# Kernel tuning notes

Hardware: AMD Instinct MI355X
Metric: run time of the kernel (lower is better)

## Reference

```python
import jax, jax.numpy as jnp
import numpy as np

B, T, C, N = 4, 1024, 960, 64
H = C // N
R_W, R_A, R_V, R_G = 64, 64, 32, 128
LN_EPS = 0.00064


def setup_inputs() -> dict:
    key = jax.random.key(0)
    ks = jax.random.split(key, 28)
    s = 0.5 / np.sqrt(C)
    u = lambda k, sh, sc: jax.random.uniform(k, sh, jnp.float32, -sc, sc)
    n = lambda k, sh, sc: jax.random.normal(k, sh, jnp.float32) * sc
    return {
        "x": jax.random.normal(ks[0], (B, T, C), jnp.float32),
        "v_first": jax.random.normal(ks[1], (B, T, C), jnp.float32),
        "x_r": jax.random.uniform(ks[2], (1, 1, C), jnp.float32),
        "x_w": jax.random.uniform(ks[3], (1, 1, C), jnp.float32),
        "x_k": jax.random.uniform(ks[4], (1, 1, C), jnp.float32),
        "x_v": jax.random.uniform(ks[5], (1, 1, C), jnp.float32),
        "x_a": jax.random.uniform(ks[6], (1, 1, C), jnp.float32),
        "x_g": jax.random.uniform(ks[7], (1, 1, C), jnp.float32),
        "w0": n(ks[8], (1, 1, C), 0.5) - 2.0,
        "w1": n(ks[9], (C, R_W), 0.02),
        "w2": n(ks[10], (R_W, C), 0.02),
        "a0": n(ks[11], (1, 1, C), 0.3),
        "a1": n(ks[12], (C, R_A), 0.02),
        "a2": n(ks[13], (R_A, C), 0.02),
        "v0": n(ks[14], (1, 1, C), 0.3) + 0.73,
        "v1": n(ks[15], (C, R_V), 0.02),
        "v2": n(ks[16], (R_V, C), 0.02),
        "g1": n(ks[17], (C, R_G), 0.02),
        "g2": n(ks[18], (R_G, C), 0.02),
        "k_k": n(ks[19], (1, 1, C), 0.1) + 0.71,
        "k_a": n(ks[20], (1, 1, C), 0.1) + 1.02,
        "r_k": n(ks[21], (H, N), 0.1) - 0.04,
        "Wr": u(ks[22], (C, C), s),
        "Wk": u(ks[23], (C, C), 0.1 * s),
        "Wv": u(ks[24], (C, C), s),
        "Wo": u(ks[25], (C, C), s),
        "ln_g": jnp.ones((C,), jnp.float32),
        "ln_b": jnp.zeros((C,), jnp.float32),
    }


def reference(x, v_first, x_r, x_w, x_k, x_v, x_a, x_g, w0, w1, w2,
              a0, a1, a2, v0, v1, v2, g1, g2, k_k, k_a, r_k,
              Wr, Wk, Wv, Wo, ln_g, ln_b):
    Bx, Tx, Cx = x.shape
    # token shift: xx[t] = x[t-1] - x[t], with x[-1] = 0
    xx = jnp.concatenate([jnp.zeros_like(x[:, :1]), x[:, :-1]], axis=1) - x
    xr = x + xx * x_r; xw = x + xx * x_w; xk = x + xx * x_k
    xv = x + xx * x_v; xa = x + xx * x_a; xg = x + xx * x_g
    r = xr @ Wr
    w_raw = w0 + jnp.tanh(xw @ w1) @ w2       # log-space decay
    k = xk @ Wk
    v = xv @ Wv
    # layer_id > 0: residual mix with layer-0 value
    v = v + (v_first - v) * jax.nn.sigmoid(v0 + (xv @ v1) @ v2)
    a = jax.nn.sigmoid(a0 + (xa @ a1) @ a2)   # in-context learning rate
    g = jax.nn.sigmoid(xg @ g1) @ g2          # gate
    kk = (k * k_k).reshape(Bx, Tx, H, N)
    kk = kk / jnp.maximum(jnp.linalg.norm(kk, axis=-1, keepdims=True), 1e-12)
    k = k * (1.0 + (a - 1.0) * k_a)
    f32 = jnp.float32
    rh = r.reshape(Bx, Tx, H, N).astype(f32)
    kh = k.reshape(Bx, Tx, H, N).astype(f32)
    vh = v.reshape(Bx, Tx, H, N).astype(f32)
    wh = jnp.exp(-jax.nn.softplus(-w_raw.reshape(Bx, Tx, H, N).astype(f32)) - 0.5)
    ah = (-kk).astype(f32)                              # removal key
    bh = (kk * a.reshape(Bx, Tx, H, N)).astype(f32)     # replacement key

    def step(state, inp):
        r_t, w_t, k_t, v_t, a_t, b_t = inp  # each (B,H,N); state (B,H,N,N)
        sa = jnp.einsum('bhij,bhj->bhi', state, a_t)
        state = (state * w_t[:, :, None, :]
                 + sa[..., None] * b_t[:, :, None, :]
                 + v_t[..., None] * k_t[:, :, None, :])
        out_t = jnp.einsum('bhij,bhj->bhi', state, r_t)
        return state, out_t

    tm = lambda u: jnp.transpose(u, (1, 0, 2, 3))  # time-major
    state0 = jnp.zeros((Bx, H, N, N), f32)
    _, wkv = jax.lax.scan(step, state0, (tm(rh), tm(wh), tm(kh), tm(vh), tm(ah), tm(bh)))
    wkv = jnp.transpose(wkv, (1, 0, 2, 3))  # (B,T,H,N)
    # GroupNorm with H groups == per-head layernorm over N
    mu = wkv.mean(-1, keepdims=True)
    var = wkv.var(-1, keepdims=True)
    xn = (wkv - mu) / jnp.sqrt(var + LN_EPS)
    xn = xn * ln_g.reshape(H, N) + ln_b.reshape(H, N)
    bonus = (rh * kh * r_k).sum(-1, keepdims=True) * vh  # r*k*v bonus term
    xo = (xn + bonus).astype(x.dtype).reshape(Bx, Tx, Cx)
    return (xo * g) @ Wo


if __name__ == "__main__":
    out = reference(**setup_inputs())
    print(out.shape, out.dtype)
```

## Files before the change

kernel.cpp:

```cpp
#include <hip/hip_runtime.h>
#include <hip/hip_bf16.h>
#include <math.h>

#define Tn 1024
#define Cn 960
#define Hn 15
#define Nn 64
#define Mn 4096

typedef short bf16x8 __attribute__((ext_vector_type(8)));
typedef float f32x4 __attribute__((ext_vector_type(4)));

#define MCc ((size_t)Mn * Cn)

__device__ __forceinline__ float sigmf(float x) { return 1.0f / (1.0f + __expf(-x)); }

__device__ __forceinline__ ushort f2bf(float x) {
    unsigned u = __float_as_uint(x);
    unsigned r = (u + 0x7FFFu + ((u >> 16) & 1u)) >> 16;
    return (ushort)r;
}
__device__ __forceinline__ float bf2f(ushort h) { return __uint_as_float(((unsigned)h) << 16); }

__device__ __forceinline__ float rowsum16(float x) {
    x += __int_as_float(__builtin_amdgcn_update_dpp(0, __float_as_int(x), 0x121, 0xF, 0xF, true));
    x += __int_as_float(__builtin_amdgcn_update_dpp(0, __float_as_int(x), 0x122, 0xF, 0xF, true));
    x += __int_as_float(__builtin_amdgcn_update_dpp(0, __float_as_int(x), 0x124, 0xF, 0xF, true));
    x += __int_as_float(__builtin_amdgcn_update_dpp(0, __float_as_int(x), 0x128, 0xF, 0xF, true));
    return x;
}

__global__ __launch_bounds__(256) void mix6_kernel(
    const float* __restrict__ x,
    const float* __restrict__ mr, const float* __restrict__ mw, const float* __restrict__ mk,
    const float* __restrict__ mv, const float* __restrict__ ma, const float* __restrict__ mg,
    ushort* __restrict__ r_sp, ushort* __restrict__ w_sp, ushort* __restrict__ k_sp,
    ushort* __restrict__ v_sp, ushort* __restrict__ a_sp, ushort* __restrict__ g_sp)
{
    int idx = blockIdx.x * 256 + threadIdx.x;
    int e = idx * 4;
    if (e >= Mn * Cn) return;
    int m = e / Cn;
    int c = e - m * Cn;
    int t = m & (Tn - 1);
    float4 xv = *(const float4*)(x + e);
    float4 xp = make_float4(0.f, 0.f, 0.f, 0.f);
    if (t > 0) xp = *(const float4*)(x + e - Cn);
    float4 dx = make_float4(xp.x - xv.x, xp.y - xv.y, xp.z - xv.z, xp.w - xv.w);
#define MIXSPLIT(MIXP, P)                                                     \
    {                                                                         \
        float4 mm = *(const float4*)(MIXP + c);                               \
        float4 O = make_float4(xv.x + dx.x * mm.x, xv.y + dx.y * mm.y,        \
                               xv.z + dx.z * mm.z, xv.w + dx.w * mm.w);       \
        ushort h0 = f2bf(O.x), h1 = f2bf(O.y), h2 = f2bf(O.z), h3 = f2bf(O.w);\
        ushort l0 = f2bf(O.x - bf2f(h0)), l1 = f2bf(O.y - bf2f(h1));          \
        ushort l2 = f2bf(O.z - bf2f(h2)), l3 = f2bf(O.w - bf2f(h3));          \
        *(ushort4*)(P + e) = make_ushort4(h0, h1, h2, h3);                    \
        *(ushort4*)(P + MCc + e) = make_ushort4(l0, l1, l2, l3);              \
    }
    MIXSPLIT(mr, r_sp)
    MIXSPLIT(mw, w_sp)
    MIXSPLIT(mk, k_sp)
    MIXSPLIT(mv, v_sp)
    MIXSPLIT(ma, a_sp)
    MIXSPLIT(mg, g_sp)
#undef MIXSPLIT
}

__global__ __launch_bounds__(256) void convWT_kernel(
    const float* __restrict__ W, ushort* __restrict__ Thi, ushort* __restrict__ Tlo)
{
    __shared__ float tile[32][33];
    int k0 = blockIdx.x * 32, n0 = blockIdx.y * 32;
    int tx = threadIdx.x & 31, ty = threadIdx.x >> 5;
#pragma unroll
    for (int i = 0; i < 4; ++i)
        tile[ty + 8 * i][tx] = W[(size_t)(k0 + ty + 8 * i) * 960 + n0 + tx];
    __syncthreads();
#pragma unroll
    for (int i = 0; i < 4; ++i) {
        float x = tile[tx][ty + 8 * i];
        ushort h = f2bf(x);
        ushort l = f2bf(x - bf2f(h));
        size_t o = (size_t)(n0 + ty + 8 * i) * 960 + k0 + tx;
        Thi[o] = h;
        Tlo[o] = l;
    }
}

__global__ __launch_bounds__(256) void wprep_kernel(
    const float* __restrict__ w1, const float* __restrict__ a1,
    const float* __restrict__ v1, const float* __restrict__ g1,
    const float* __restrict__ w2, const float* __restrict__ a2,
    const float* __restrict__ v2, const float* __restrict__ g2,
    ushort* __restrict__ arena)
{
    __shared__ float tile[32][33];
    int z = blockIdx.z;
    const float* src;
    int K, N;
    size_t off;
    switch (z) {
        case 0: src = w1; K = 960; N = 64;  off = 0;      break;
        case 1: src = a1; K = 960; N = 64;  off = 122880; break;
        case 2: src = v1; K = 960; N = 32;  off = 245760; break;
        case 3: src = g1; K = 960; N = 128; off = 307200; break;
        case 4: src = w2; K = 64;  N = 960; off = 552960; break;
        case 5: src = a2; K = 64;  N = 960; off = 675840; break;
        case 6: src = v2; K = 32;  N = 960; off = 798720; break;
        default: src = g2; K = 128; N = 960; off = 860160; break;
    }
    int k0 = blockIdx.x * 32, n0 = blockIdx.y * 32;
    if (k0 >= K || n0 >= N) return;
    int tx = threadIdx.x & 31, ty = threadIdx.x >> 5;
#pragma unroll
    for (int i = 0; i < 4; ++i)
        tile[ty + 8 * i][tx] = src[(size_t)(k0 + ty + 8 * i) * N + n0 + tx];
    __syncthreads();
    ushort* Thi = arena + off;
    ushort* Tlo = arena + off + (size_t)K * N;
#pragma unroll
    for (int i = 0; i < 4; ++i) {
        float x = tile[tx][ty + 8 * i];
        ushort h = f2bf(x);
        ushort l = f2bf(x - bf2f(h));
        size_t o = (size_t)(n0 + ty + 8 * i) * K + k0 + tx;
        Thi[o] = h;
        Tlo[o] = l;
    }
}

__global__ __launch_bounds__(256) void convN_kernel(
    const float* __restrict__ X, ushort* __restrict__ hi, ushort* __restrict__ lo, int n4)
{
    int idx = blockIdx.x * 256 + threadIdx.x;
    if (idx >= n4) return;
    int e = idx * 4;
    float4 x = *(const float4*)(X + e);
    ushort h0 = f2bf(x.x), h1 = f2bf(x.y), h2 = f2bf(x.z), h3 = f2bf(x.w);
    ushort l0 = f2bf(x.x - bf2f(h0)), l1 = f2bf(x.y - bf2f(h1));
    ushort l2 = f2bf(x.z - bf2f(h2)), l3 = f2bf(x.w - bf2f(h3));
    *(ushort4*)(hi + e) = make_ushort4(h0, h1, h2, h3);
    *(ushort4*)(lo + e) = make_ushort4(l0, l1, l2, l3);
}

__global__ __launch_bounds__(512) void gemm_bf3_kernel(
    const ushort* __restrict__ Ahi, const ushort* __restrict__ Alo,
    const ushort* __restrict__ Bhi, const ushort* __restrict__ Blo,
    float* __restrict__ C, int ldc)
{
    __shared__ __align__(16) ushort sA[2][2][128][40];
    __shared__ __align__(16) ushort sB[2][2][64][40];
    const int K = 960;
    int bm = blockIdx.x * 128, bn = blockIdx.y * 64;
    int t = threadIdx.x;
    int w = t >> 6, l = t & 63;
    int lr = l & 15, lk = l >> 4;

    int ar = t >> 2, aseg = t & 3;
    int brr = t >> 2;
    int bhl = brr >> 6, brow = brr & 63, bseg = t & 3;
    const ushort* gAh = Ahi + (size_t)(bm + ar) * K + aseg * 8;
    const ushort* gAl = Alo + (size_t)(bm + ar) * K + aseg * 8;
    const ushort* gB = (bhl ? Blo : Bhi) + (size_t)(bn + brow) * K + bseg * 8;

    f32x4 acc[4];
#pragma unroll
    for (int j = 0; j < 4; ++j)
#pragma unroll
        for (int e = 0; e < 4; ++e) acc[j][e] = 0.f;

    float4 rhP, rlP, rbP, rhQ, rlQ, rbQ;
#define LOADP(KOFF)                                                           \
    {                                                                         \
        rhP = *(const float4*)(gAh + (KOFF));                                 \
        rlP = *(const float4*)(gAl + (KOFF));                                 \
        rbP = *(const float4*)(gB + (KOFF));                                  \
    }
#define LOADQ(KOFF)                                                           \
    {                                                                         \
        rhQ = *(const float4*)(gAh + (KOFF));                                 \
        rlQ = *(const float4*)(gAl + (KOFF));                                 \
        rbQ = *(const float4*)(gB + (KOFF));                                  \
    }
#define WRITEP(BUF)                                                           \
    {                                                                         \
        *(float4*)&sA[BUF][0][ar][aseg * 8] = rhP;                            \
        *(float4*)&sA[BUF][1][ar][aseg * 8] = rlP;                            \
        *(float4*)&sB[BUF][bhl][brow][bseg * 8] = rbP;                        \
    }
#define WRITEQ(BUF)                                                           \
    {                                                                         \
        *(float4*)&sA[BUF][0][ar][aseg * 8] = rhQ;                            \
        *(float4*)&sA[BUF][1][ar][aseg * 8] = rlQ;                            \
        *(float4*)&sB[BUF][bhl][brow][bseg * 8] = rbQ;                        \
    }
#define COMPUTEK(BUF)                                                         \
    {                                                                         \
        bf16x8 ah, al, bh[4], bl[4];                                          \
        ah = *(const bf16x8*)&sA[BUF][0][16 * w + lr][lk * 8];                \
        al = *(const bf16x8*)&sA[BUF][1][16 * w + lr][lk * 8];                \
        _Pragma("unroll")                                                     \
        for (int j = 0; j < 4; ++j) {                                         \
            bh[j] = *(const bf16x8*)&sB[BUF][0][16 * j + lr][lk * 8];         \
            bl[j] = *(const bf16x8*)&sB[BUF][1][16 * j + lr][lk * 8];         \
        }                                                                     \
        _Pragma("unroll")                                                     \
        for (int j = 0; j < 4; ++j) {                                         \
            acc[j] = __builtin_amdgcn_mfma_f32_16x16x32_bf16(ah, bh[j], acc[j], 0, 0, 0); \
            acc[j] = __builtin_amdgcn_mfma_f32_16x16x32_bf16(ah, bl[j], acc[j], 0, 0, 0); \
            acc[j] = __builtin_amdgcn_mfma_f32_16x16x32_bf16(al, bh[j], acc[j], 0, 0, 0); \
        }                                                                     \
    }

    LOADP(0)
    WRITEP(0)
    LOADQ(32)
    asm volatile("s_waitcnt lgkmcnt(0)" ::: "memory");
    __builtin_amdgcn_s_barrier();

    int cur = 0;
    for (int ks = 0; ks < 30; ks += 2) {
        int k2 = (ks + 2 < 30 ? ks + 2 : 29) * 32;
        LOADP(k2)
        COMPUTEK(cur)
        WRITEQ(cur ^ 1)
        asm volatile("s_waitcnt lgkmcnt(0)" ::: "memory");
        __builtin_amdgcn_s_barrier();
        cur ^= 1;
        int k3 = (ks + 3 < 30 ? ks + 3 : 29) * 32;
        LOADQ(k3)
        COMPUTEK(cur)
        WRITEP(cur ^ 1)
        asm volatile("s_waitcnt lgkmcnt(0)" ::: "memory");
        __builtin_amdgcn_s_barrier();
        cur ^= 1;
    }

#pragma unroll
    for (int j = 0; j < 4; ++j)
#pragma unroll
        for (int jr = 0; jr < 4; ++jr) {
            int row = bm + 16 * w + lk * 4 + jr;
            int col = bn + 16 * j + lr;
            C[(size_t)row * ldc + col] = acc[j][jr];
        }
#undef COMPUTEK
#undef WRITEP
#undef WRITEQ
#undef LOADP
#undef LOADQ
}

__device__ __forceinline__ void lora_core(
    const ushort* __restrict__ Ahi, const ushort* __restrict__ Alo, int lda,
    const ushort* __restrict__ Bhi, const ushort* __restrict__ Blo,
    float* __restrict__ C, int ldc, int Nvalid, int K, int act, int bn)
{
    __shared__ __align__(16) ushort sA[2][2][128][40];
    __shared__ __align__(16) ushort sB[2][2][64][40];
    int bm = blockIdx.x * 128;
    int t = threadIdx.x;
    int w = t >> 6, l = t & 63;
    int lr = l & 15, lk = l >> 4;

    int ar = t >> 2, aseg = t & 3;
    int brr = t >> 2;
    int bhl = brr >> 6, brow = brr & 63, bseg = t & 3;
    const ushort* gAh = Ahi + (size_t)(bm + ar) * lda + aseg * 8;
    const ushort* gAl = Alo + (size_t)(bm + ar) * lda + aseg * 8;
    const ushort* gB = (bhl ? Blo : Bhi) + (size_t)(bn + brow) * K + bseg * 8;

    f32x4 acc[4];
#pragma unroll
    for (int j = 0; j < 4; ++j)
#pragma unroll
        for (int e = 0; e < 4; ++e) acc[j][e] = 0.f;

    float4 rhP, rlP, rbP, rhQ, rlQ, rbQ;
#define LLOADP(KOFF)                                                          \
    {                                                                         \
        rhP = *(const float4*)(gAh + (KOFF));                                 \
        rlP = *(const float4*)(gAl + (KOFF));                                 \
        rbP = *(const float4*)(gB + (KOFF));                                  \
    }
#define LLOADQ(KOFF)                                                          \
    {                                                                         \
        rhQ = *(const float4*)(gAh + (KOFF));                                 \
        rlQ = *(const float4*)(gAl + (KOFF));                                 \
        rbQ = *(const float4*)(gB + (KOFF));                                  \
    }
#define LWRITEP(BUF)                                                          \
    {                                                                         \
        *(float4*)&sA[BUF][0][ar][aseg * 8] = rhP;                            \
        *(float4*)&sA[BUF][1][ar][aseg * 8] = rlP;                            \
        *(float4*)&sB[BUF][bhl][brow][bseg * 8] = rbP;                        \
    }
#define LWRITEQ(BUF)                                                          \
    {                                                                         \
        *(float4*)&sA[BUF][0][ar][aseg * 8] = rhQ;                            \
        *(float4*)&sA[BUF][1][ar][aseg * 8] = rlQ;                            \
        *(float4*)&sB[BUF][bhl][brow][bseg * 8] = rbQ;                        \
    }
#define LCOMPUTE(BUF)                                                         \
// ... 46 lines not shown
                else if (act == 2) v = sigmf(v);
                C[(size_t)row * ldc + col] = v;
            }
        }
#undef LCOMPUTE
#undef LWRITEP
#undef LWRITEQ
#undef LLOADP
#undef LLOADQ
}

__global__ __launch_bounds__(512) void lora_down_kernel(
    const ushort* __restrict__ xw_sp, const ushort* __restrict__ xa_sp,
    const ushort* __restrict__ xv_sp, const ushort* __restrict__ xg_sp,
    const ushort* __restrict__ arena, float* __restrict__ hid)
{
    int z = blockIdx.z;
    int bn = blockIdx.y * 64;
    const ushort* A;
    size_t off;
    int N, act, coff;
    switch (z) {
        case 0: A = xw_sp; off = 0;      N = 64;  act = 1; coff = 0;   break;
        case 1: A = xa_sp; off = 122880; N = 64;  act = 0; coff = 64;  break;
        case 2: A = xv_sp; off = 245760; N = 32;  act = 0; coff = 128; break;
        default: A = xg_sp; off = 307200; N = 128; act = 2; coff = 160; break;
    }
    if (bn >= N) return;
    lora_core(A, A + MCc, Cn, arena + off, arena + off + (size_t)960 * N,
              hid + coff, 288, N, 960, act, bn);
}

__global__ __launch_bounds__(512) void lora_up_kernel(
    const ushort* __restrict__ hidHi, const ushort* __restrict__ hidLo,
    const ushort* __restrict__ arena,
    float* __restrict__ oW, float* __restrict__ oA,
    float* __restrict__ oV, float* __restrict__ oG)
{
    int z = blockIdx.z;
    int bn = blockIdx.y * 64;
    size_t off;
    int K, aoff;
    float* C;
    switch (z) {
        case 0: off = 552960; K = 64;  aoff = 0;   C = oW; break;
        case 1: off = 675840; K = 64;  aoff = 64;  C = oA; break;
        case 2: off = 798720; K = 32;  aoff = 128; C = oV; break;
        default: off = 860160; K = 128; aoff = 160; C = oG; break;
    }
    lora_core(hidHi + aoff, hidLo + aoff, 288, arena + off,
              arena + off + (size_t)K * 960, C, Cn, Cn, K, 0, bn);
}

__global__ __launch_bounds__(256, 2) void scan_kernel(
    const float* __restrict__ rP, const float* __restrict__ wrawP,
    const float* __restrict__ apreP, const float* __restrict__ vsigP,
    const float* __restrict__ krawP, const float* __restrict__ vrawP,
    const float* __restrict__ vfirstP, const float* __restrict__ gP,
    const float* __restrict__ w0, const float* __restrict__ a0,
    const float* __restrict__ v0c, const float* __restrict__ kkc,
    const float* __restrict__ kac, const float* __restrict__ r_k,
    const float* __restrict__ ln_g, const float* __restrict__ ln_b,
    ushort* __restrict__ xsp)
{
    __shared__ float buf[2][7][16][64];
    __shared__ float outL[16][64];
    int tid = threadIdx.x;
    int q = tid >> 6, l = tid & 63;
    int blk = blockIdx.x;
    int bh = blk >> 3, seg = blk & 7;
    int bb = bh / Hn, h = bh - bb * Hn;
    size_t base = (size_t)bb * Tn * Cn + h * 64;
    int rg = l >> 4, cg = l & 15;
    int row0 = 16 * q + 4 * rg;
    int c0 = 4 * cg;

    int sstep = tid >> 4, sseg = tid & 15;
    size_t soff = base + (size_t)sstep * Cn + sseg * 4;
    int wofs = sstep * 64 + sseg * 4;
    int ccol = h * 64 + sseg * 4;

    int cbeg = (seg == 0) ? 0 : 8 * seg - 4;
    int cendc = 8 * seg + 8;
    int coutc = 8 * seg;

    float4 w0c4 = *(const float4*)(w0 + ccol);
    float4 a0c4 = *(const float4*)(a0 + ccol);
    float4 v0c4 = *(const float4*)(v0c + ccol);
    float4 kkc4 = *(const float4*)(kkc + ccol);
    float4 kac4 = *(const float4*)(kac + ccol);
    float4 rk4 = *(const float4*)(r_k + ccol);
    float4 lg4 = *(const float4*)(ln_g + ccol);
    float4 lb4 = *(const float4*)(ln_b + ccol);

    float s[4][4];
#pragma unroll
    for (int r = 0; r < 4; ++r)
#pragma unroll
        for (int c = 0; c < 4; ++c) s[r][c] = 0.f;

    float4 g_r, g_wr, g_vr, g_vf, g_vs, g_g, g_kr, g_ap;

#define LOADSTAGE(OFF)                                                        \
    g_r = *(const float4*)(rP + soff + (OFF));                                \
    g_wr = *(const float4*)(wrawP + soff + (OFF));                            \
    g_vr = *(const float4*)(vrawP + soff + (OFF));                            \
    g_vf = *(const float4*)(vfirstP + soff + (OFF));                          \
    g_vs = *(const float4*)(vsigP + soff + (OFF));                            \
    g_g = *(const float4*)(gP + soff + (OFF));                                \
    g_kr = *(const float4*)(krawP + soff + (OFF));                            \
    g_ap = *(const float4*)(apreP + soff + (OFF));

#define PARK(BN)                                                              \
    {                                                                         \
        const float E = 0.60653065971263342f;                                 \
        float4 w4;                                                            \
        w4.x = sigmf(w0c4.x + g_wr.x) * E;                                    \
        w4.y = sigmf(w0c4.y + g_wr.y) * E;                                    \
        w4.z = sigmf(w0c4.z + g_wr.z) * E;                                    \
        w4.w = sigmf(w0c4.w + g_wr.w) * E;                                    \
        float4 v4;                                                            \
        v4.x = g_vr.x + (g_vf.x - g_vr.x) * sigmf(v0c4.x + g_vs.x);           \
        v4.y = g_vr.y + (g_vf.y - g_vr.y) * sigmf(v0c4.y + g_vs.y);           \
        v4.z = g_vr.z + (g_vf.z - g_vr.z) * sigmf(v0c4.z + g_vs.z);           \
        v4.w = g_vr.w + (g_vf.w - g_vr.w) * sigmf(v0c4.w + g_vs.w);           \
        float4 a4;                                                            \
        a4.x = sigmf(a0c4.x + g_ap.x);                                        \
        a4.y = sigmf(a0c4.y + g_ap.y);                                        \
        a4.z = sigmf(a0c4.z + g_ap.z);                                        \
        a4.w = sigmf(a0c4.w + g_ap.w);                                        \
        float4 kk;                                                            \
        kk.x = g_kr.x * kkc4.x; kk.y = g_kr.y * kkc4.y;                       \
        kk.z = g_kr.z * kkc4.z; kk.w = g_kr.w * kkc4.w;                       \
        float ss = kk.x * kk.x + kk.y * kk.y + kk.z * kk.z + kk.w * kk.w;     \
        ss = rowsum16(ss);                                                    \
        float inv = 1.0f / fmaxf(sqrtf(ss), 1e-12f);                          \
        float4 ah4, bh4, kh4;                                                 \
        ah4.x = -kk.x * inv; bh4.x = kk.x * inv * a4.x;                       \
        ah4.y = -kk.y * inv; bh4.y = kk.y * inv * a4.y;                       \
        ah4.z = -kk.z * inv; bh4.z = kk.z * inv * a4.z;                       \
        ah4.w = -kk.w * inv; bh4.w = kk.w * inv * a4.w;                       \
        kh4.x = g_kr.x * (1.0f + (a4.x - 1.0f) * kac4.x);                     \
        kh4.y = g_kr.y * (1.0f + (a4.y - 1.0f) * kac4.y);                     \
        kh4.z = g_kr.z * (1.0f + (a4.z - 1.0f) * kac4.z);                     \
        kh4.w = g_kr.w * (1.0f + (a4.w - 1.0f) * kac4.w);                     \
        *(float4*)((BN) + 0 * 1024 + wofs) = g_r;                             \
        *(float4*)((BN) + 1 * 1024 + wofs) = w4;                              \
        *(float4*)((BN) + 2 * 1024 + wofs) = kh4;                             \
        *(float4*)((BN) + 3 * 1024 + wofs) = ah4;                             \
        *(float4*)((BN) + 4 * 1024 + wofs) = bh4;                             \
        *(float4*)((BN) + 5 * 1024 + wofs) = v4;                              \
        *(float4*)((BN) + 6 * 1024 + wofs) = g_g;                             \
    }

    LOADSTAGE((size_t)cbeg * 16 * Cn)
    PARK(&buf[0][0][0][0])
    asm volatile("s_waitcnt lgkmcnt(0)" ::: "memory");
    __builtin_amdgcn_s_barrier();

#define DECL2(S)                                                              \
    float4 S##a0, S##w0, S##k0, S##b0, S##r0, S##v0;                          \
    float4 S##a1, S##w1, S##k1, S##b1, S##r1, S##v1;
#define DSLOAD2(S, T)                                                         \
    S##a0 = *(const float4*)(bc + 3 * 1024 + (T) * 64 + c0);                  \
    S##w0 = *(const float4*)(bc + 1 * 1024 + (T) * 64 + c0);                  \
    S##k0 = *(const float4*)(bc + 2 * 1024 + (T) * 64 + c0);                  \
    S##b0 = *(const float4*)(bc + 4 * 1024 + (T) * 64 + c0);                  \
    S##r0 = *(const float4*)(bc + 0 * 1024 + (T) * 64 + c0);                  \
    S##v0 = *(const float4*)(bc + 5 * 1024 + (T) * 64 + row0);                \
    S##a1 = *(const float4*)(bc + 3 * 1024 + ((T) + 1) * 64 + c0);            \
    S##w1 = *(const float4*)(bc + 1 * 1024 + ((T) + 1) * 64 + c0);            \
    S##k1 = *(const float4*)(bc + 2 * 1024 + ((T) + 1) * 64 + c0);            \
    S##b1 = *(const float4*)(bc + 4 * 1024 + ((T) + 1) * 64 + c0);            \
    S##r1 = *(const float4*)(bc + 0 * 1024 + ((T) + 1) * 64 + c0);            \
    S##v1 = *(const float4*)(bc + 5 * 1024 + ((T) + 1) * 64 + row0);
#define STEP(AV, WV, KV, BV, RV, VV, T)                                       \
    {                                                                         \
        float sp0 = s[0][0] * AV.x + s[0][1] * AV.y + s[0][2] * AV.z + s[0][3] * AV.w; \
        float sp1 = s[1][0] * AV.x + s[1][1] * AV.y + s[1][2] * AV.z + s[1][3] * AV.w; \
        float sp2 = s[2][0] * AV.x + s[2][1] * AV.y + s[2][2] * AV.z + s[2][3] * AV.w; \
        float sp3 = s[3][0] * AV.x + s[3][1] * AV.y + s[3][2] * AV.z + s[3][3] * AV.w; \
        sp0 = rowsum16(sp0);                                                  \
        sp1 = rowsum16(sp1);                                                  \
        sp2 = rowsum16(sp2);                                                  \
        sp3 = rowsum16(sp3);                                                  \
        float sa[4] = {sp0, sp1, sp2, sp3};                                   \
        float vr[4] = {VV.x, VV.y, VV.z, VV.w};                               \
        float op[4];                                                          \
        _Pragma("unroll")                                                     \
        for (int r = 0; r < 4; ++r) {                                         \
            s[r][0] = s[r][0] * WV.x + sa[r] * BV.x + vr[r] * KV.x;           \
            float o = s[r][0] * RV.x;                                         \
            s[r][1] = s[r][1] * WV.y + sa[r] * BV.y + vr[r] * KV.y;           \
            o += s[r][1] * RV.y;                                              \
            s[r][2] = s[r][2] * WV.z + sa[r] * BV.z + vr[r] * KV.z;           \
            o += s[r][2] * RV.z;                                              \
            s[r][3] = s[r][3] * WV.w + sa[r] * BV.w + vr[r] * KV.w;           \
            o += s[r][3] * RV.w;                                              \
            op[r] = rowsum16(o);                                              \
        }                                                                     \
        if (cg == 0)                                                          \
            *(float4*)&outL[T][row0] = make_float4(op[0], op[1], op[2], op[3]); \
    }

    DECL2(A) DECL2(B)

    int cur = 0;
    for (int c = cbeg; c < cendc; ++c) {
        const float* bc = &buf[cur][0][0][0];
        {
            int cnxt = (c + 1 < cendc) ? c + 1 : c;
            LOADSTAGE((size_t)cnxt * 16 * Cn)
        }

        DSLOAD2(A, 0)
#pragma unroll
        for (int it = 0; it < 4; ++it) {
            DSLOAD2(B, 4 * it + 2)
            STEP(Aa0, Aw0, Ak0, Ab0, Ar0, Av0, 4 * it + 0)
            STEP(Aa1, Aw1, Ak1, Ab1, Ar1, Av1, 4 * it + 1)
            if (it < 3) { DSLOAD2(A, 4 * it + 4) }
            STEP(Ba0, Bw0, Bk0, Bb0, Br0, Bv0, 4 * it + 2)
            STEP(Ba1, Bw1, Bk1, Bb1, Br1, Bv1, 4 * it + 3)
        }

        PARK(&buf[cur ^ 1][0][0][0])
        asm volatile("s_waitcnt lgkmcnt(0)" ::: "memory");
        __builtin_amdgcn_s_barrier();

        if (c >= coutc) {
            float4 o4 = *(const float4*)&outL[sstep][4 * sseg];
            float4 r4 = *(const float4*)(bc + 0 * 1024 + sstep * 64 + 4 * sseg);
            float4 k4 = *(const float4*)(bc + 2 * 1024 + sstep * 64 + 4 * sseg);
            float4 v4 = *(const float4*)(bc + 5 * 1024 + sstep * 64 + 4 * sseg);
            float4 gg4 = *(const float4*)(bc + 6 * 1024 + sstep * 64 + 4 * sseg);
            float m1 = o4.x + o4.y + o4.z + o4.w;
            float m2 = o4.x * o4.x + o4.y * o4.y + o4.z * o4.z + o4.w * o4.w;
            float bd = r4.x * k4.x * rk4.x + r4.y * k4.y * rk4.y +
                       r4.z * k4.z * rk4.z + r4.w * k4.w * rk4.w;
            m1 = rowsum16(m1);
            m2 = rowsum16(m2);
            bd = rowsum16(bd);
            float mean = m1 * (1.f / 64.f);
            float var = m2 * (1.f / 64.f) - mean * mean;
            float is = rsqrtf(var + 0.00064f);
            float xo0 = ((o4.x - mean) * is * lg4.x + lb4.x + bd * v4.x) * gg4.x;
            float xo1 = ((o4.y - mean) * is * lg4.y + lb4.y + bd * v4.y) * gg4.y;
            float xo2 = ((o4.z - mean) * is * lg4.z + lb4.z + bd * v4.z) * gg4.z;
            float xo3 = ((o4.w - mean) * is * lg4.w + lb4.w + bd * v4.w) * gg4.w;
            ushort h0 = f2bf(xo0), h1 = f2bf(xo1), h2 = f2bf(xo2), h3 = f2bf(xo3);
            ushort l0 = f2bf(xo0 - bf2f(h0)), l1 = f2bf(xo1 - bf2f(h1));
            ushort l2 = f2bf(xo2 - bf2f(h2)), l3 = f2bf(xo3 - bf2f(h3));
            size_t gt = (size_t)c * 16 + sstep;
            size_t eo = base + gt * Cn + 4 * sseg;
            *(ushort4*)(xsp + eo) = make_ushort4(h0, h1, h2, h3);
            *(ushort4*)(xsp + MCc + eo) = make_ushort4(l0, l1, l2, l3);
        }
        __builtin_amdgcn_s_barrier();
        cur ^= 1;
    }
#undef STEP
#undef DSLOAD2
#undef DECL2
#undef PARK
#undef LOADSTAGE
}

extern "C" void kernel_launch(void* const* d_in, const int* in_sizes, int n_in,
                              void* d_out, int out_size, void* d_ws, size_t ws_size,
                              hipStream_t stream)
{
    const float* x       = (const float*)d_in[0];
    const float* v_first = (const float*)d_in[1];
    const float* x_r     = (const float*)d_in[2];
    const float* x_w     = (const float*)d_in[3];
    const float* x_k     = (const float*)d_in[4];
    const float* x_v     = (const float*)d_in[5];
    const float* x_a     = (const float*)d_in[6];
    const float* x_g     = (const float*)d_in[7];
    const float* w0      = (const float*)d_in[8];
    const float* w1      = (const float*)d_in[9];
    const float* w2      = (const float*)d_in[10];
    const float* a0      = (const float*)d_in[11];
    const float* a1      = (const float*)d_in[12];
    const float* a2      = (const float*)d_in[13];
    const float* v0c     = (const float*)d_in[14];
    const float* v1      = (const float*)d_in[15];
    const float* v2      = (const float*)d_in[16];
    const float* g1w     = (const float*)d_in[17];
    const float* g2w     = (const float*)d_in[18];
    const float* k_k     = (const float*)d_in[19];
    const float* k_a     = (const float*)d_in[20];
    const float* r_k     = (const float*)d_in[21];
    const float* Wr      = (const float*)d_in[22];
    const float* Wk      = (const float*)d_in[23];
    const float* Wv      = (const float*)d_in[24];
    const float* Wo      = (const float*)d_in[25];
    const float* ln_g    = (const float*)d_in[26];
    const float* ln_b    = (const float*)d_in[27];
    float* out = (float*)d_out;

    float* ws = (float*)d_ws;
    float* B0 = ws + 0 * MCc;
    float* B1 = ws + 1 * MCc;
    float* B2 = ws + 2 * MCc;
    float* B3 = ws + 3 * MCc;
    float* B4 = ws + 4 * MCc;
    float* B5 = ws + 5 * MCc;
    float* B6 = ws + 6 * MCc;
    float* B7 = ws + 7 * MCc;
    float* B8 = ws + 8 * MCc;
    float* hid = ws + 9 * MCc;

    ushort* XRsp = (ushort*)B0;
    ushort* XWsp = (ushort*)B1;
    ushort* XKsp = (ushort*)B2;
    ushort* XVsp = (ushort*)out;
    ushort* XAsp = (ushort*)B4;
    ushort* XGsp = (ushort*)B5;
    ushort* S3 = (ushort*)B3;
    ushort* hidHi = S3;
    ushort* hidLo = S3 + 1179648;
    ushort* arena = S3 + 2359296;
    ushort* Whi = (ushort*)hid;
    ushort* Wlo = Whi + (size_t)960 * 960;
    ushort* Xsp = (ushort*)B4;

    mix6_kernel<<<3840, 256, 0, stream>>>(x, x_r, x_w, x_k, x_v, x_a, x_g,
                                          XRsp, XWsp, XKsp, XVsp, XAsp, XGsp);
    wprep_kernel<<<dim3(30, 30, 8), 256, 0, stream>>>(w1, a1, v1, g1w,
                                                      w2, a2, v2, g2w, arena);

    dim3 gW(30, 30);
    dim3 gM(32, 15);
    convWT_kernel<<<gW, 256, 0, stream>>>(Wr, Whi, Wlo);
    gemm_bf3_kernel<<<gM, 512, 0, stream>>>(XRsp, XRsp + MCc, Whi, Wlo, B6, Cn);
    convWT_kernel<<<gW, 256, 0, stream>>>(Wk, Whi, Wlo);
    gemm_bf3_kernel<<<gM, 512, 0, stream>>>(XKsp, XKsp + MCc, Whi, Wlo, B7, Cn);
    convWT_kernel<<<gW, 256, 0, stream>>>(Wv, Whi, Wlo);
    gemm_bf3_kernel<<<gM, 512, 0, stream>>>(XVsp, XVsp + MCc, Whi, Wlo, B8, Cn);

    lora_down_kernel<<<dim3(32, 2, 4), 512, 0, stream>>>(XWsp, XAsp, XVsp, XGsp,
                                                         arena, hid);
    convN_kernel<<<1152, 256, 0, stream>>>(hid, hidHi, hidLo, Mn * 288 / 4);
    lora_up_kernel<<<dim3(32, 15, 4), 512, 0, stream>>>(hidHi, hidLo, arena,
                                                        B0, B2, B1, B5);
    convWT_kernel<<<gW, 256, 0, stream>>>(Wo, Whi, Wlo);
    scan_kernel<<<480, 256, 0, stream>>>(B6, B0, B2, B1, B7, B8, v_first, B5,
                                         w0, a0, v0c, k_k, k_a,
                                         r_k, ln_g, ln_b, Xsp);
    gemm_bf3_kernel<<<gM, 512, 0, stream>>>(Xsp, Xsp + MCc, Whi, Wlo, out, Cn);
}
```

Before: 340.1 us.

## Batch R/K/V projections into one launch, retile GEMM, split scan finer

The three weight conversions and the three projection GEMMs are each merged into one z-indexed launch, with each converted weight kept in its own workspace slot. The GEMM block drops from 512 to 256 threads, and each wave now computes two 16-row tiles, which gives more register-level reuse per wave. The scan kernel splits each head's time range into 16 chunks of 8 steps instead of 8 chunks of 16, doubling the grid and raising launch bounds to 4 waves. The trade-off is more redundant warm-up recomputation per scan chunk and higher register pressure in the GEMM.

Measured after the change: 462.4 us. +36.0%, slower.

```diff
diff --git a/kernel.cpp b/kernel.cpp
--- a/kernel.cpp
+++ b/kernel.cpp
@@ -71,6 +71,33 @@
     const float* __restrict__ W, ushort* __restrict__ Thi, ushort* __restrict__ Tlo)
 {
     __shared__ float tile[32][33];
+    int k0 = blockIdx.x * 32, n0 = blockIdx.y * 32;
+    int tx = threadIdx.x & 31, ty = threadIdx.x >> 5;
+#pragma unroll
+    for (int i = 0; i < 4; ++i)
+        tile[ty + 8 * i][tx] = W[(size_t)(k0 + ty + 8 * i) * 960 + n0 + tx];
+    __syncthreads();
+#pragma unroll
+    for (int i = 0; i < 4; ++i) {
+        float x = tile[tx][ty + 8 * i];
+        ushort h = f2bf(x);
+        ushort l = f2bf(x - bf2f(h));
+        size_t o = (size_t)(n0 + ty + 8 * i) * 960 + k0 + tx;
+        Thi[o] = h;
+        Tlo[o] = l;
+    }
+}
+
+__global__ __launch_bounds__(256) void convWT3_kernel(
+    const float* __restrict__ Wr, const float* __restrict__ Wk,
+    const float* __restrict__ Wv,
+    ushort* __restrict__ S0, ushort* __restrict__ S1, ushort* __restrict__ S2)
+{
+    __shared__ float tile[32][33];
+    int z = blockIdx.z;
+    const float* W = (z == 0) ? Wr : (z == 1) ? Wk : Wv;
+    ushort* Thi = (z == 0) ? S0 : (z == 1) ? S1 : S2;
+    ushort* Tlo = Thi + (size_t)960 * 960;
     int k0 = blockIdx.x * 32, n0 = blockIdx.y * 32;
     int tx = threadIdx.x & 31, ty = threadIdx.x >> 5;
 #pragma unroll
@@ -144,73 +171,94 @@
     *(ushort4*)(lo + e) = make_ushort4(l0, l1, l2, l3);
 }
 
-__global__ __launch_bounds__(512) void gemm_bf3_kernel(
+__device__ __forceinline__ void gemm_core(
     const ushort* __restrict__ Ahi, const ushort* __restrict__ Alo,
     const ushort* __restrict__ Bhi, const ushort* __restrict__ Blo,
-    float* __restrict__ C, int ldc)
+    float* __restrict__ C, int ldc, int bm, int bn)
 {
     __shared__ __align__(16) ushort sA[2][2][128][40];
     __shared__ __align__(16) ushort sB[2][2][64][40];
     const int K = 960;
-    int bm = blockIdx.x * 128, bn = blockIdx.y * 64;
     int t = threadIdx.x;
     int w = t >> 6, l = t & 63;
     int lr = l & 15, lk = l >> 4;
 
-    int ar = t >> 2, aseg = t & 3;
-    int brr = t >> 2;
-    int bhl = brr >> 6, brow = brr & 63, bseg = t & 3;
-    const ushort* gAh = Ahi + (size_t)(bm + ar) * K + aseg * 8;
-    const ushort* gAl = Alo + (size_t)(bm + ar) * K + aseg * 8;
-    const ushort* gB = (bhl ? Blo : Bhi) + (size_t)(bn + brow) * K + bseg * 8;
-
-    f32x4 acc[4];
-#pragma unroll
-    for (int j = 0; j < 4; ++j)
-#pragma unroll
-        for (int e = 0; e < 4; ++e) acc[j][e] = 0.f;
-
-    float4 rhP, rlP, rbP, rhQ, rlQ, rbQ;
+    int ar = t >> 1, aseg = t & 1;
+    int br = t & 63, bhalf = (t >> 6) & 1, bseg = t >> 7;
+    const ushort* gAh = Ahi + (size_t)(bm + ar) * K + aseg * 16;
+    const ushort* gAl = Alo + (size_t)(bm + ar) * K + aseg * 16;
+    const ushort* gB = (bhalf ? Blo : Bhi) + (size_t)(bn + br) * K + bseg * 16;
+
+    f32x4 acc[2][4];
+#pragma unroll
+    for (int i = 0; i < 2; ++i)
+#pragma unroll
+        for (int j = 0; j < 4; ++j)
+#pragma unroll
+            for (int e = 0; e < 4; ++e) acc[i][j][e] = 0.f;
+
+    float4 h0P, h1P, l0P, l1P, b0P, b1P;
+    float4 h0Q, h1Q, l0Q, l1Q, b0Q, b1Q;
 #define LOADP(KOFF)                                                           \
     {                                                                         \
-        rhP = *(const float4*)(gAh + (KOFF));                                 \
-        rlP = *(const float4*)(gAl + (KOFF));                                 \
-        rbP = *(const float4*)(gB + (KOFF));                                  \
+        h0P = *(const float4*)(gAh + (KOFF));                                 \
+        h1P = *(const float4*)(gAh + (KOFF) + 8);                             \
+        l0P = *(const float4*)(gAl + (KOFF));                                 \
+        l1P = *(const float4*)(gAl + (KOFF) + 8);                             \
+        b0P = *(const float4*)(gB + (KOFF));                                  \
+        b1P = *(const float4*)(gB + (KOFF) + 8);                              \
     }
 #define LOADQ(KOFF)                                                           \
     {                                                                         \
-        rhQ = *(const float4*)(gAh + (KOFF));                                 \
-        rlQ = *(const float4*)(gAl + (KOFF));                                 \
-        rbQ = *(const float4*)(gB + (KOFF));                                  \
+        h0Q = *(const float4*)(gAh + (KOFF));                                 \
+        h1Q = *(const float4*)(gAh + (KOFF) + 8);                             \
+        l0Q = *(const float4*)(gAl + (KOFF));                                 \
+        l1Q = *(const float4*)(gAl + (KOFF) + 8);                             \
+        b0Q = *(const float4*)(gB + (KOFF));                                  \
+        b1Q = *(const float4*)(gB + (KOFF) + 8);                              \
     }
 #define WRITEP(BUF)                                                           \
     {                                                                         \
-        *(float4*)&sA[BUF][0][ar][aseg * 8] = rhP;                            \
-        *(float4*)&sA[BUF][1][ar][aseg * 8] = rlP;                            \
-        *(float4*)&sB[BUF][bhl][brow][bseg * 8] = rbP;                        \
+        *(float4*)&sA[BUF][0][ar][aseg * 16] = h0P;                           \
+        *(float4*)&sA[BUF][0][ar][aseg * 16 + 8] = h1P;                       \
+        *(float4*)&sA[BUF][1][ar][aseg * 16] = l0P;                           \
+        *(float4*)&sA[BUF][1][ar][aseg * 16 + 8] = l1P;                       \
+        *(float4*)&sB[BUF][bhalf][br][bseg * 16] = b0P;                       \
+        *(float4*)&sB[BUF][bhalf][br][bseg * 16 + 8] = b1P;                   \
     }
 #define WRITEQ(BUF)                                                           \
     {                                                                         \
-        *(float4*)&sA[BUF][0][ar][aseg * 8] = rhQ;                            \
-        *(float4*)&sA[BUF][1][ar][aseg * 8] = rlQ;                            \
-        *(float4*)&sB[BUF][bhl][brow][bseg * 8] = rbQ;                        \
+        *(float4*)&sA[BUF][0][ar][aseg * 16] = h0Q;                           \
+        *(float4*)&sA[BUF][0][ar][aseg * 16 + 8] = h1Q;                       \
+        *(float4*)&sA[BUF][1][ar][aseg * 16] = l0Q;                           \
+        *(float4*)&sA[BUF][1][ar][aseg * 16 + 8] = l1Q;                       \
+        *(float4*)&sB[BUF][bhalf][br][bseg * 16] = b0Q;                       \
+        *(float4*)&sB[BUF][bhalf][br][bseg * 16 + 8] = b1Q;                   \
     }
 #define COMPUTEK(BUF)                                                         \
     {                                                                         \
-        bf16x8 ah, al, bh[4], bl[4];                                          \
-        ah = *(const bf16x8*)&sA[BUF][0][16 * w + lr][lk * 8];                \
-        al = *(const bf16x8*)&sA[BUF][1][16 * w + lr][lk * 8];                \
+        bf16x8 ah[2], al[2], bh[4], bl[4];                                    \
+        _Pragma("unroll")                                                     \
+        for (int i = 0; i < 2; ++i) {                                         \
+            ah[i] = *(const bf16x8*)&sA[BUF][0][32 * w + 16 * i + lr][lk * 8];\
+            al[i] = *(const bf16x8*)&sA[BUF][1][32 * w + 16 * i + lr][lk * 8];\
+        }                                                                     \
         _Pragma("unroll")                                                     \
         for (int j = 0; j < 4; ++j) {                                         \
             bh[j] = *(const bf16x8*)&sB[BUF][0][16 * j + lr][lk * 8];         \
             bl[j] = *(const bf16x8*)&sB[BUF][1][16 * j + lr][lk * 8];         \
         }                                                                     \
         _Pragma("unroll")                                                     \
-        for (int j = 0; j < 4; ++j) {                                         \
-            acc[j] = __builtin_amdgcn_mfma_f32_16x16x32_bf16(ah, bh[j], acc[j], 0, 0, 0); \
-            acc[j] = __builtin_amdgcn_mfma_f32_16x16x32_bf16(ah, bl[j], acc[j], 0, 0, 0); \
-            acc[j] = __builtin_amdgcn_mfma_f32_16x16x32_bf16(al, bh[j], acc[j], 0, 0, 0); \
-        }                                                                     \
+        for (int i = 0; i < 2; ++i)                                           \
+            _Pragma("unroll")                                                 \
+            for (int j = 0; j < 4; ++j) {                                     \
+                acc[i][j] = __builtin_amdgcn_mfma_f32_16x16x32_bf16(          \
+                    ah[i], bh[j], acc[i][j], 0, 0, 0);                        \
+                acc[i][j] = __builtin_amdgcn_mfma_f32_16x16x32_bf16(          \
+                    ah[i], bl[j], acc[i][j], 0, 0, 0);                        \
+                acc[i][j] = __builtin_amdgcn_mfma_f32_16x16x32_bf16(          \
+                    al[i], bh[j], acc[i][j], 0, 0, 0);                        \
+            }                                                                 \
     }
 
     LOADP(0)
@@ -238,18 +286,43 @@
     }
 
 #pragma unroll
-    for (int j = 0; j < 4; ++j)
-#pragma unroll
-        for (int jr = 0; jr < 4; ++jr) {
-            int row = bm + 16 * w + lk * 4 + jr;
-            int col = bn + 16 * j + lr;
-            C[(size_t)row * ldc + col] = acc[j][jr];
-        }
+    for (int i = 0; i < 2; ++i)
+#pragma unroll
+        for (int j = 0; j < 4; ++j)
+#pragma unroll
+            for (int jr = 0; jr < 4; ++jr) {
+                int row = bm + 32 * w + 16 * i + lk * 4 + jr;
+                int col = bn + 16 * j + lr;
+                C[(size_t)row * ldc + col] = acc[i][j][jr];
+            }
 #undef COMPUTEK
 #undef WRITEP
 #undef WRITEQ
 #undef LOADP
 #undef LOADQ
+}
+
+__global__ __launch_bounds__(256) void gemm3_kernel(
+    const ushort* __restrict__ XR, const ushort* __restrict__ XK,
+    const ushort* __restrict__ XV,
+    const ushort* __restrict__ WrS, const ushort* __restrict__ WkS,
+    const ushort* __restrict__ WvS,
+    float* __restrict__ oR, float* __restrict__ oK, float* __restrict__ oV)
+{
+    int z = blockIdx.z;
+    const ushort* A = (z == 0) ? XR : (z == 1) ? XK : XV;
+    const ushort* W = (z == 0) ? WrS : (z == 1) ? WkS : WvS;
+    float* C = (z == 0) ? oR : (z == 1) ? oK : oV;
+    gemm_core(A, A + MCc, W, W + (size_t)960 * 960, C, Cn,
+              blockIdx.x * 128, blockIdx.y * 64);
+}
+
+__global__ __launch_bounds__(256) void gemm1_kernel(
+    const ushort* __restrict__ Ahi, const ushort* __restrict__ Alo,
+    const ushort* __restrict__ Bhi, const ushort* __restrict__ Blo,
+    float* __restrict__ C, int ldc)
+{
+    gemm_core(Ahi, Alo, Bhi, Blo, C, ldc, blockIdx.x * 128, blockIdx.y * 64);
 }
 
 __device__ __forceinline__ void lora_core(
@@ -402,7 +475,7 @@
               arena + off + (size_t)K * 960, C, Cn, Cn, K, 0, bn);
 }
 
-__global__ __launch_bounds__(256, 2) void scan_kernel(
+__global__ __launch_bounds__(256, 4) void scan_kernel(
     const float* __restrict__ rP, const float* __restrict__ wrawP,
     const float* __restrict__ apreP, const float* __restrict__ vsigP,
     const float* __restrict__ krawP, const float* __restrict__ vrawP,
@@ -413,35 +486,35 @@
     const float* __restrict__ ln_g, const float* __restrict__ ln_b,
     ushort* __restrict__ xsp)
 {
-    __shared__ float buf[2][7][16][64];
-    __shared__ float outL[16][64];
+    __shared__ float buf[2][7][8][64];
+    __shared__ float outL[8][64];
     int tid = threadIdx.x;
     int q = tid >> 6, l = tid & 63;
     int blk = blockIdx.x;
-    int bh = blk >> 3, seg = blk & 7;
+    int bh = blk >> 4, seg = blk & 15;
     int bb = bh / Hn, h = bh - bb * Hn;
     size_t base = (size_t)bb * Tn * Cn + h * 64;
     int rg = l >> 4, cg = l & 15;
     int row0 = 16 * q + 4 * rg;
     int c0 = 4 * cg;
 
-    int sstep = tid >> 4, sseg = tid & 15;
-    size_t soff = base + (size_t)sstep * Cn + sseg * 4;
-    int wofs = sstep * 64 + sseg * 4;
-    int ccol = h * 64 + sseg * 4;
-
-    int cbeg = (seg == 0) ? 0 : 8 * seg - 4;
+    int sstep = tid >> 5, sseg = tid & 31;
+    size_t soff = base + (size_t)sstep * Cn + sseg * 2;
+    int wofs = sstep * 64 + sseg * 2;
+    int ccol = h * 64 + sseg * 2;
+
+    int cbeg = (seg == 0) ? 0 : 8 * seg - 8;
     int cendc = 8 * seg + 8;
     int coutc = 8 * seg;
 
-    float4 w0c4 = *(const float4*)(w0 + ccol);
-    float4 a0c4 = *(const float4*)(a0 + ccol);
-    float4 v0c4 = *(const float4*)(v0c + ccol);
-    float4 kkc4 = *(const float4*)(kkc + ccol);
-    float4 kac4 = *(const float4*)(kac + ccol);
-    float4 rk4 = *(const float4*)(r_k + ccol);
-    float4 lg4 = *(const float4*)(ln_g + ccol);
-    float4 lb4 = *(const float4*)(ln_b + ccol);
+    float2 w0c2 = *(const float2*)(w0 + ccol);
+    float2 a0c2 = *(const float2*)(a0 + ccol);
+    float2 v0c2 = *(const float2*)(v0c + ccol);
+    float2 kkc2 = *(const float2*)(kkc + ccol);
+    float2 kac2 = *(const float2*)(kac + ccol);
+    float2 rk2 = *(const float2*)(r_k + ccol);
+    float2 lg2 = *(const float2*)(ln_g + ccol);
+    float2 lb2 = *(const float2*)(ln_b + ccol);
 
     float s[4][4];
 #pragma unroll
@@ -449,61 +522,51 @@
 #pragma unroll
         for (int c = 0; c < 4; ++c) s[r][c] = 0.f;
 
-    float4 g_r, g_wr, g_vr, g_vf, g_vs, g_g, g_kr, g_ap;
+    float2 g_r, g_wr, g_vr, g_vf, g_vs, g_g, g_kr, g_ap;
 
 #define LOADSTAGE(OFF)                                                        \
-    g_r = *(const float4*)(rP + soff + (OFF));                                \
-    g_wr = *(const float4*)(wrawP + soff + (OFF));                            \
-    g_vr = *(const float4*)(vrawP + soff + (OFF));                            \
-    g_vf = *(const float4*)(vfirstP + soff + (OFF));                          \
-    g_vs = *(const float4*)(vsigP + soff + (OFF));                            \
-    g_g = *(const float4*)(gP + soff + (OFF));                                \
-    g_kr = *(const float4*)(krawP + soff + (OFF));                            \
-    g_ap = *(const float4*)(apreP + soff + (OFF));
+    g_r = *(const float2*)(rP + soff + (OFF));                                \
+    g_wr = *(const float2*)(wrawP + soff + (OFF));                            \
+    g_vr = *(const float2*)(vrawP + soff + (OFF));                            \
+    g_vf = *(const float2*)(vfirstP + soff + (OFF));                          \
+    g_vs = *(const float2*)(vsigP + soff + (OFF));                            \
+    g_g = *(const float2*)(gP + soff + (OFF));                                \
+    g_kr = *(const float2*)(krawP + soff + (OFF));                            \
+    g_ap = *(const float2*)(apreP + soff + (OFF));
 
 #define PARK(BN)                                                              \
     {                                                                         \
         const float E = 0.60653065971263342f;                                 \
-        float4 w4;                                                            \
-        w4.x = sigmf(w0c4.x + g_wr.x) * E;                                    \
-        w4.y = sigmf(w0c4.y + g_wr.y) * E;                                    \
-        w4.z = sigmf(w0c4.z + g_wr.z) * E;                                    \
-        w4.w = sigmf(w0c4.w + g_wr.w) * E;                                    \
-        float4 v4;                                                            \
-        v4.x = g_vr.x + (g_vf.x - g_vr.x) * sigmf(v0c4.x + g_vs.x);           \
-        v4.y = g_vr.y + (g_vf.y - g_vr.y) * sigmf(v0c4.y + g_vs.y);           \
-        v4.z = g_vr.z + (g_vf.z - g_vr.z) * sigmf(v0c4.z + g_vs.z);           \
-        v4.w = g_vr.w + (g_vf.w - g_vr.w) * sigmf(v0c4.w + g_vs.w);           \
-        float4 a4;                                                            \
-        a4.x = sigmf(a0c4.x + g_ap.x);                                        \
-        a4.y = sigmf(a0c4.y + g_ap.y);                                        \
-        a4.z = sigmf(a0c4.z + g_ap.z);                                        \
-        a4.w = sigmf(a0c4.w + g_ap.w);                                        \
-        float4 kk;                                                            \
-        kk.x = g_kr.x * kkc4.x; kk.y = g_kr.y * kkc4.y;                       \
-        kk.z = g_kr.z * kkc4.z; kk.w = g_kr.w * kkc4.w;                       \
-        float ss = kk.x * kk.x + kk.y * kk.y + kk.z * kk.z + kk.w * kk.w;     \
+        float2 w2;                                                            \
+        w2.x = sigmf(w0c2.x + g_wr.x) * E;                                    \
+        w2.y = sigmf(w0c2.y + g_wr.y) * E;                                    \
+        float2 v2;                                                            \
+        v2.x = g_vr.x + (g_vf.x - g_vr.x) * sigmf(v0c2.x + g_vs.x);           \
+        v2.y = g_vr.y + (g_vf.y - g_vr.y) * sigmf(v0c2.y + g_vs.y);           \
+        float2 a2;                                                            \
+        a2.x = sigmf(a0c2.x + g_ap.x);                                        \
+        a2.y = sigmf(a0c2.y + g_ap.y);                                        \
+        float2 kk;                                                            \
+        kk.x = g_kr.x * kkc2.x; kk.y = g_kr.y * kkc2.y;                       \
+        float ss = kk.x * kk.x + kk.y * kk.y;                                 \
         ss = rowsum16(ss);                                                    \
+        ss += __shfl_xor(ss, 16);                                             \
         float inv = 1.0f / fmaxf(sqrtf(ss), 1e-12f);                          \
-        float4 ah4, bh4, kh4;                                                 \
-        ah4.x = -kk.x * inv; bh4.x = kk.x * inv * a4.x;                       \
-        ah4.y = -kk.y * inv; bh4.y = kk.y * inv * a4.y;                       \
-        ah4.z = -kk.z * inv; bh4.z = kk.z * inv * a4.z;                       \
-        ah4.w = -kk.w * inv; bh4.w = kk.w * inv * a4.w;                       \
-        kh4.x = g_kr.x * (1.0f + (a4.x - 1.0f) * kac4.x);                     \
-        kh4.y = g_kr.y * (1.0f + (a4.y - 1.0f) * kac4.y);                     \
-        kh4.z = g_kr.z * (1.0f + (a4.z - 1.0f) * kac4.z);                     \
-        kh4.w = g_kr.w * (1.0f + (a4.w - 1.0f) * kac4.w);                     \
-        *(float4*)((BN) + 0 * 1024 + wofs) = g_r;                             \
-        *(float4*)((BN) + 1 * 1024 + wofs) = w4;                              \
-        *(float4*)((BN) + 2 * 1024 + wofs) = kh4;                             \
-        *(float4*)((BN) + 3 * 1024 + wofs) = ah4;                             \
-        *(float4*)((BN) + 4 * 1024 + wofs) = bh4;                             \
-        *(float4*)((BN) + 5 * 1024 + wofs) = v4;                              \
-        *(float4*)((BN) + 6 * 1024 + wofs) = g_g;                             \
-    }
-
-    LOADSTAGE((size_t)cbeg * 16 * Cn)
+        float2 ah2, bh2, kh2;                                                 \
+        ah2.x = -kk.x * inv; bh2.x = kk.x * inv * a2.x;                       \
+        ah2.y = -kk.y * inv; bh2.y = kk.y * inv * a2.y;                       \
+        kh2.x = g_kr.x * (1.0f + (a2.x - 1.0f) * kac2.x);                     \
+        kh2.y = g_kr.y * (1.0f + (a2.y - 1.0f) * kac2.y);                     \
+        *(float2*)((BN) + 0 * 512 + wofs) = g_r;                              \
+        *(float2*)((BN) + 1 * 512 + wofs) = w2;                               \
+        *(float2*)((BN) + 2 * 512 + wofs) = kh2;                              \
+        *(float2*)((BN) + 3 * 512 + wofs) = ah2;                              \
+        *(float2*)((BN) + 4 * 512 + wofs) = bh2;                              \
+        *(float2*)((BN) + 5 * 512 + wofs) = v2;                               \
+        *(float2*)((BN) + 6 * 512 + wofs) = g_g;                              \
+    }
+
+    LOADSTAGE((size_t)cbeg * 8 * Cn)
     PARK(&buf[0][0][0][0])
     asm volatile("s_waitcnt lgkmcnt(0)" ::: "memory");
     __builtin_amdgcn_s_barrier();
@@ -512,18 +575,18 @@
     float4 S##a0, S##w0, S##k0, S##b0, S##r0, S##v0;                          \
     float4 S##a1, S##w1, S##k1, S##b1, S##r1, S##v1;
 #define DSLOAD2(S, T)                                                         \
-    S##a0 = *(const float4*)(bc + 3 * 1024 + (T) * 64 + c0);                  \
-    S##w0 = *(const float4*)(bc + 1 * 1024 + (T) * 64 + c0);                  \
-    S##k0 = *(const float4*)(bc + 2 * 1024 + (T) * 64 + c0);                  \
-    S##b0 = *(const float4*)(bc + 4 * 1024 + (T) * 64 + c0);                  \
-    S##r0 = *(const float4*)(bc + 0 * 1024 + (T) * 64 + c0);                  \
-    S##v0 = *(const float4*)(bc + 5 * 1024 + (T) * 64 + row0);                \
-    S##a1 = *(const float4*)(bc + 3 * 1024 + ((T) + 1) * 64 + c0);            \
-    S##w1 = *(const float4*)(bc + 1 * 1024 + ((T) + 1) * 64 + c0);            \
-    S##k1 = *(const float4*)(bc + 2 * 1024 + ((T) + 1) * 64 + c0);            \
-    S##b1 = *(const float4*)(bc + 4 * 1024 + ((T) + 1) * 64 + c0);            \
-    S##r1 = *(const float4*)(bc + 0 * 1024 + ((T) + 1) * 64 + c0);            \
-    S##v1 = *(const float4*)(bc + 5 * 1024 + ((T) + 1) * 64 + row0);
+    S##a0 = *(const float4*)(bc + 3 * 512 + (T) * 64 + c0);                   \
+    S##w0 = *(const float4*)(bc + 1 * 512 + (T) * 64 + c0);                   \
+    S##k0 = *(const float4*)(bc + 2 * 512 + (T) * 64 + c0);                   \
+    S##b0 = *(const float4*)(bc + 4 * 512 + (T) * 64 + c0);                   \
+    S##r0 = *(const float4*)(bc + 0 * 512 + (T) * 64 + c0);                   \
+    S##v0 = *(const float4*)(bc + 5 * 512 + (T) * 64 + row0);                 \
+    S##a1 = *(const float4*)(bc + 3 * 512 + ((T) + 1) * 64 + c0);             \
+    S##w1 = *(const float4*)(bc + 1 * 512 + ((T) + 1) * 64 + c0);             \
+    S##k1 = *(const float4*)(bc + 2 * 512 + ((T) + 1) * 64 + c0);             \
+    S##b1 = *(const float4*)(bc + 4 * 512 + ((T) + 1) * 64 + c0);             \
+    S##r1 = *(const float4*)(bc + 0 * 512 + ((T) + 1) * 64 + c0);             \
+    S##v1 = *(const float4*)(bc + 5 * 512 + ((T) + 1) * 64 + row0);
 #define STEP(AV, WV, KV, BV, RV, VV, T)                                       \
     {                                                                         \
         float sp0 = s[0][0] * AV.x + s[0][1] * AV.y + s[0][2] * AV.z + s[0][3] * AV.w; \
@@ -560,16 +623,16 @@
         const float* bc = &buf[cur][0][0][0];
         {
             int cnxt = (c + 1 < cendc) ? c + 1 : c;
-            LOADSTAGE((size_t)cnxt * 16 * Cn)
+            LOADSTAGE((size_t)cnxt * 8 * Cn)
         }
 
         DSLOAD2(A, 0)
 #pragma unroll
-        for (int it = 0; it < 4; ++it) {
+        for (int it = 0; it < 2; ++it) {
             DSLOAD2(B, 4 * it + 2)
             STEP(Aa0, Aw0, Ak0, Ab0, Ar0, Av0, 4 * it + 0)
             STEP(Aa1, Aw1, Ak1, Ab1, Ar1, Av1, 4 * it + 1)
-            if (it < 3) { DSLOAD2(A, 4 * it + 4) }
+            if (it < 1) { DSLOAD2(A, 4 * it + 4) }
             STEP(Ba0, Bw0, Bk0, Bb0, Br0, Bv0, 4 * it + 2)
             STEP(Ba1, Bw1, Bk1, Bb1, Br1, Bv1, 4 * it + 3)
         }
@@ -579,32 +642,28 @@
         __builtin_amdgcn_s_barrier();
 
         if (c >= coutc) {
-            float4 o4 = *(const float4*)&outL[sstep][4 * sseg];
-            float4 r4 = *(const float4*)(bc + 0 * 1024 + sstep * 64 + 4 * sseg);
-            float4 k4 = *(const float4*)(bc + 2 * 1024 + sstep * 64 + 4 * sseg);
-            float4 v4 = *(const float4*)(bc + 5 * 1024 + sstep * 64 + 4 * sseg);
-            float4 gg4 = *(const float4*)(bc + 6 * 1024 + sstep * 64 + 4 * sseg);
-            float m1 = o4.x + o4.y + o4.z + o4.w;
-            float m2 = o4.x * o4.x + o4.y * o4.y + o4.z * o4.z + o4.w * o4.w;
-            float bd = r4.x * k4.x * rk4.x + r4.y * k4.y * rk4.y +
-                       r4.z * k4.z * rk4.z + r4.w * k4.w * rk4.w;
-            m1 = rowsum16(m1);
-            m2 = rowsum16(m2);
-            bd = rowsum16(bd);
+            float2 o2 = *(const float2*)&outL[sstep][2 * sseg];
+            float2 r2 = *(const float2*)(bc + 0 * 512 + sstep * 64 + 2 * sseg);
+            float2 k2 = *(const float2*)(bc + 2 * 512 + sstep * 64 + 2 * sseg);
+            float2 v2 = *(const float2*)(bc + 5 * 512 + sstep * 64 + 2 * sseg);
+            float2 gg2 = *(const float2*)(bc + 6 * 512 + sstep * 64 + 2 * sseg);
+            float m1 = o2.x + o2.y;
+            float m2 = o2.x * o2.x + o2.y * o2.y;
+            float bd = r2.x * k2.x * rk2.x + r2.y * k2.y * rk2.y;
+            m1 = rowsum16(m1); m1 += __shfl_xor(m1, 16);
+            m2 = rowsum16(m2); m2 += __shfl_xor(m2, 16);
+            bd = rowsum16(bd); bd += __shfl_xor(bd, 16);
             float mean = m1 * (1.f / 64.f);
             float var = m2 * (1.f / 64.f) - mean * mean;
             float is = rsqrtf(var + 0.00064f);
-            float xo0 = ((o4.x - mean) * is * lg4.x + lb4.x + bd * v4.x) * gg4.x;
-            float xo1 = ((o4.y - mean) * is * lg4.y + lb4.y + bd * v4.y) * gg4.y;
-            float xo2 = ((o4.z - mean) * is * lg4.z + lb4.z + bd * v4.z) * gg4.z;
-            float xo3 = ((o4.w - mean) * is * lg4.w + lb4.w + bd * v4.w) * gg4.w;
-            ushort h0 = f2bf(xo0), h1 = f2bf(xo1), h2 = f2bf(xo2), h3 = f2bf(xo3);
+            float xo0 = ((o2.x - mean) * is * lg2.x + lb2.x + bd * v2.x) * gg2.x;
+            float xo1 = ((o2.y - mean) * is * lg2.y + lb2.y + bd * v2.y) * gg2.y;
+            ushort h0 = f2bf(xo0), h1 = f2bf(xo1);
             ushort l0 = f2bf(xo0 - bf2f(h0)), l1 = f2bf(xo1 - bf2f(h1));
-            ushort l2 = f2bf(xo2 - bf2f(h2)), l3 = f2bf(xo3 - bf2f(h3));
-            size_t gt = (size_t)c * 16 + sstep;
-            size_t eo = base + gt * Cn + 4 * sseg;
-            *(ushort4*)(xsp + eo) = make_ushort4(h0, h1, h2, h3);
-            *(ushort4*)(xsp + MCc + eo) = make_ushort4(l0, l1, l2, l3);
+            size_t gt = (size_t)c * 8 + sstep;
+            size_t eo = base + gt * Cn + 2 * sseg;
+            *(ushort2*)(xsp + eo) = make_ushort2(h0, h1);
+            *(ushort2*)(xsp + MCc + eo) = make_ushort2(l0, l1);
         }
         __builtin_amdgcn_s_barrier();
         cur ^= 1;
@@ -672,6 +731,9 @@
     ushort* hidHi = S3;
     ushort* hidLo = S3 + 1179648;
     ushort* arena = S3 + 2359296;
+    ushort* WkS = S3 + 3465216;
+    ushort* WvS = S3 + 5308416;
+    ushort* WrS = (ushort*)hid;
     ushort* Whi = (ushort*)hid;
     ushort* Wlo = Whi + (size_t)960 * 960;
     ushort* Xsp = (ushort*)B4;
@@ -680,24 +742,20 @@
                                           XRsp, XWsp, XKsp, XVsp, XAsp, XGsp);
     wprep_kernel<<<dim3(30, 30, 8), 256, 0, stream>>>(w1, a1, v1, g1w,
                                                       w2, a2, v2, g2w, arena);
-
-    dim3 gW(30, 30);
-    dim3 gM(32, 15);
-    convWT_kernel<<<gW, 256, 0, stream>>>(Wr, Whi, Wlo);
-    gemm_bf3_kernel<<<gM, 512, 0, stream>>>(XRsp, XRsp + MCc, Whi, Wlo, B6, Cn);
-    convWT_kernel<<<gW, 256, 0, stream>>>(Wk, Whi, Wlo);
-    gemm_bf3_kernel<<<gM, 512, 0, stream>>>(XKsp, XKsp + MCc, Whi, Wlo, B7, Cn);
-    convWT_kernel<<<gW, 256, 0, stream>>>(Wv, Whi, Wlo);
-    gemm_bf3_kernel<<<gM, 512, 0, stream>>>(XVsp, XVsp + MCc, Whi, Wlo, B8, Cn);
-
+    convWT3_kernel<<<dim3(30, 30, 3), 256, 0, stream>>>(Wr, Wk, Wv,
+                                                        WrS, WkS, WvS);
+    gemm3_kernel<<<dim3(32, 15, 3), 256, 0, stream>>>(XRsp, XKsp, XVsp,
+                                                      WrS, WkS, WvS,
+                                                      B6, B7, B8);
     lora_down_kernel<<<dim3(32, 2, 4), 512, 0, stream>>>(XWsp, XAsp, XVsp, XGsp,
                                                          arena, hid);
     convN_kernel<<<1152, 256, 0, stream>>>(hid, hidHi, hidLo, Mn * 288 / 4);
     lora_up_kernel<<<dim3(32, 15, 4), 512, 0, stream>>>(hidHi, hidLo, arena,
                                                         B0, B2, B1, B5);
-    convWT_kernel<<<gW, 256, 0, stream>>>(Wo, Whi, Wlo);
-    scan_kernel<<<480, 256, 0, stream>>>(B6, B0, B2, B1, B7, B8, v_first, B5,
+    convWT_kernel<<<dim3(30, 30), 256, 0, stream>>>(Wo, Whi, Wlo);
+    scan_kernel<<<960, 256, 0, stream>>>(B6, B0, B2, B1, B7, B8, v_first, B5,
                                          w0, a0, v0c, k_k, k_a,
                                          r_k, ln_g, ln_b, Xsp);
-    gemm_bf3_kernel<<<gM, 512, 0, stream>>>(Xsp, Xsp + MCc, Whi, Wlo, out, Cn);
-}
+    gemm1_kernel<<<dim3(32, 15), 256, 0, stream>>>(Xsp, Xsp + MCc, Whi, Wlo,
+                                                   out, Cn);
+}
```
